# Optimization experiments

Measured on AMD Instinct MI355X. Metric: run time of the kernel, lower is better.

## Reference

```python
import jax, jax.numpy as jnp
import numpy as np

B, T, F, U, L, C = 1024, 100, 300, 512, 2, 10
EPS = 1e-3  # keras LayerNormalization default epsilon


def _ln(z, g, b):
    m = jnp.mean(z, axis=-1, keepdims=True)
    v = jnp.var(z, axis=-1, keepdims=True)
    return (z - m) * jax.lax.rsqrt(v + EPS) * g + b


def _cell(xt, h, c, W, R, bias, kg, kb, rg, rb, sg, sb):
    # LayerNormLSTMCell: LN(x@W) + LN(h@R) + b, gates i,f,g,o; LN on new cell state
    z = _ln(xt @ W, kg, kb) + _ln(h @ R, rg, rb) + bias
    i, f, g, o = jnp.split(z, 4, axis=-1)
    c_new = jax.nn.sigmoid(f) * c + jax.nn.sigmoid(i) * jnp.tanh(g)
    c_new = _ln(c_new, sg, sb)
    h_new = jax.nn.sigmoid(o) * jnp.tanh(c_new)
    return h_new, c_new


def setup_inputs() -> dict:
    key = jax.random.key(0)
    ks = jax.random.split(key, 8 + 2 * L)
    d = {}
    d["x"] = jax.random.normal(ks[0], (B, T, F), jnp.float32)
    lens = jax.random.randint(ks[1], (B,), 1, T + 1)
    d["mask"] = (jnp.arange(T)[None, :] < lens[:, None]).astype(jnp.int32)
    in_dims = [F, U]
    ki = 2
    for l in range(L):
        s = 1.0 / np.sqrt(in_dims[l])
        d[f"W{l}"] = jax.random.uniform(ks[ki], (in_dims[l], 4 * U), jnp.float32, -s, s); ki += 1
        d[f"R{l}"] = jax.random.uniform(ks[ki], (U, 4 * U), jnp.float32, -0.044, 0.044); ki += 1
        d[f"b{l}"] = jnp.zeros((4 * U,), jnp.float32)
        d[f"kg{l}"] = jnp.ones((4 * U,), jnp.float32)
        d[f"kb{l}"] = jnp.zeros((4 * U,), jnp.float32)
        d[f"rg{l}"] = jnp.ones((4 * U,), jnp.float32)
        d[f"rb{l}"] = jnp.zeros((4 * U,), jnp.float32)
        d[f"sg{l}"] = jnp.ones((U,), jnp.float32)
        d[f"sb{l}"] = jnp.zeros((U,), jnp.float32)
    s = 1.0 / np.sqrt(U)
    d["Wd"] = jax.random.uniform(ks[ki], (U, C), jnp.float32, -s, s)
    d["bd"] = jnp.zeros((C,), jnp.float32)
    return d


def _forward(x, mask,
             W0, R0, b0, kg0, kb0, rg0, rb0, sg0, sb0,
             W1, R1, b1, kg1, kb1, rg1, rb1, sg1, sb1,
             Wd, bd):
    params = [
        (W0, R0, b0, kg0, kb0, rg0, rb0, sg0, sb0),
        (W1, R1, b1, kg1, kb1, rg1, rb1, sg1, sb1),
    ]
    bsz = x.shape[0]
    dt = x.dtype

    def step(carry, inp_t):
        states, out_prev = carry
        xt, mt = inp_t  # xt: [B,F], mt: [B] bool
        mb = mt[:, None]
        inp = xt
        new_states = []
        for (h, c), p in zip(states, params):
            hn, cn = _cell(inp, h, c, *p)
            inp = hn
            # Keras RNN masking: carry previous state at masked steps
            new_states.append((jnp.where(mb, hn, h), jnp.where(mb, cn, c)))
        out = jnp.where(mb, inp, out_prev)
        return (tuple(new_states), out), None

    init_states = tuple((jnp.zeros((bsz, U), dt), jnp.zeros((bsz, U), dt)) for _ in range(L))
    carry0 = (init_states, jnp.zeros((bsz, U), dt))
    xs = (jnp.transpose(x, (1, 0, 2)), mask.T.astype(bool))  # time-major
    (_, out), _ = jax.lax.scan(step, carry0, xs)
    return jax.nn.softmax(out @ Wd + bd, axis=-1)


def reference(x, mask,
              W0, R0, b0, kg0, kb0, rg0, rb0, sg0, sb0,
              W1, R1, b1, kg1, kb1, rg1, rb1, sg1, sb1,
              Wd, bd):
    return _forward(x, mask,
                    W0, R0, b0, kg0, kb0, rg0, rb0, sg0, sb0,
                    W1, R1, b1, kg1, kb1, rg1, rb1, sg1, sb1,
                    Wd, bd)
```

## Files before the change

kernel.cpp:

```cpp
#include <hip/hip_runtime.h>

#define B_ 1024
#define T_ 100
#define F_ 300
#define FP_ 320
#define U_ 512
#define G4_ 2048
#define C_ 10
#define EPS_ 1e-3f

typedef _Float16 f16x8 __attribute__((ext_vector_type(8)));
typedef float f32x4 __attribute__((ext_vector_type(4)));

typedef __attribute__((address_space(1))) const void* gcptr_t;
typedef __attribute__((address_space(3))) void* lptr_t;

__device__ __forceinline__ void async_ld16(_Float16* lds, const _Float16* g) {
  __builtin_amdgcn_global_load_lds((gcptr_t)g, (lptr_t)lds, 16, 0, 0);
}

__global__ __launch_bounds__(1024) void prep_kernel(const int* __restrict__ mask,
                                                    int* __restrict__ perm,
                                                    int* __restrict__ nt) {
  __shared__ int cnt[T_ + 1];
  __shared__ int start[T_ + 1];
  int b = threadIdx.x;
  if (b <= T_) cnt[b] = 0;
  __syncthreads();
  const int* mrow = mask + (size_t)b * T_;
  int len = 0;
  for (int t = 0; t < T_; t++) len += mrow[t];
  atomicAdd(&cnt[len], 1);
  __syncthreads();
  if (b == 0) {
    int run = 0;
    for (int l = T_; l >= 0; l--) {
      start[l] = run;
      run += cnt[l];
    }
  }
  __syncthreads();
  if (b < T_) nt[b] = start[b];
  __syncthreads();
  int pos = atomicAdd(&start[len], 1);
  perm[pos] = b;
}


__global__ __launch_bounds__(256) void cast_x_kernel(const float* __restrict__ x,
                                                     const int* __restrict__ perm,
                                                     const int* __restrict__ nt,
                                                     _Float16* __restrict__ xhi,
                                                     _Float16* __restrict__ xlo) {
  size_t cidx = (size_t)blockIdx.x * 256 + threadIdx.x;
  int fc = (int)(cidx % (FP_ / 8));
  size_t bt = cidx / (FP_ / 8);
  int i = (int)(bt % B_);
  int t = (int)(bt / B_);
  int nr = (nt[t] + 127) & ~127;
  if (i >= nr) return;
  int b = perm[i];
  int f = fc * 8;
  const float* xr = x + ((size_t)b * T_ + t) * F_;
  float v[8];
  if (f + 8 <= F_) {
    float4 a = *(const float4*)(xr + f);
    float4 c = *(const float4*)(xr + f + 4);
    v[0] = a.x; v[1] = a.y; v[2] = a.z; v[3] = a.w;
    v[4] = c.x; v[5] = c.y; v[6] = c.z; v[7] = c.w;
  } else {
#pragma unroll
    for (int j = 0; j < 8; j++) v[j] = (f + j < F_) ? xr[f + j] : 0.f;
  }
  f16x8 hi, lo;
#pragma unroll
  for (int j = 0; j < 8; j++) {
    _Float16 h = (_Float16)v[j];
    hi[j] = h;
    lo[j] = (_Float16)(v[j] - (float)h);
  }
  *(f16x8*)(xhi + cidx * 8) = hi;
  *(f16x8*)(xlo + cidx * 8) = lo;
}

__global__ __launch_bounds__(256) void cast_w_kernel(const float* __restrict__ W,
                                                     _Float16* __restrict__ Whi,
                                                     _Float16* __restrict__ Wlo,
                                                     int K, int N, int Kp) {
  __shared__ float tile[32][33];
  int n0 = blockIdx.x * 32, k0 = blockIdx.y * 32;
  int tx = threadIdx.x & 31, ty = threadIdx.x >> 5;
#pragma unroll
  for (int r = 0; r < 32; r += 8) {
    int k = k0 + ty + r;
    tile[ty + r][tx] = (k < K) ? W[(size_t)k * N + n0 + tx] : 0.f;
  }
  __syncthreads();
#pragma unroll
  for (int r = 0; r < 32; r += 8) {
    int n = n0 + ty + r, kk = k0 + tx;
    if (kk < Kp) {
      float v = tile[tx][ty + r];
      _Float16 h = (_Float16)v;
      Whi[(size_t)n * Kp + kk] = h;
      Wlo[(size_t)n * Kp + kk] = (_Float16)(v - (float)h);
    }
  }
}

struct GemmOp {
  const _Float16* A;
  const _Float16* Bt;
  float* G;
  int lda;
  int K;
  size_t aLo;
  int step;
};
struct G4Pack {
  GemmOp op[4];
  const int* nt;
};

__global__ __launch_bounds__(256) void gemm_phase(G4Pack P) {
  GemmOp op = P.op[blockIdx.z];
  const int mBase = blockIdx.y * 128, nBase = blockIdx.x * 128;
  if (mBase >= P.nt[op.step]) return;
  const int K = op.K, lda = op.lda;
  const _Float16* Ah = op.A;
  const _Float16* Al = op.A + op.aLo;
  const _Float16* Bh = op.Bt;
  const _Float16* Bl = op.Bt + (size_t)G4_ * K;

  __shared__ __align__(16) _Float16 ash[128][64];
  __shared__ __align__(16) _Float16 asl[128][64];
  __shared__ __align__(16) _Float16 bsh[128][64];
  __shared__ __align__(16) _Float16 bsl[128][64];

  const int tid = threadIdx.x;
  const int w = tid >> 6;
  const int lane = tid & 63;
  const int wm = (w & 1) << 6;
  const int wn = (w >> 1) << 6;

  f32x4 acc[4][4];
#pragma unroll
  for (int mt = 0; mt < 4; mt++)
#pragma unroll
    for (int nt2 = 0; nt2 < 4; nt2++) acc[mt][nt2] = (f32x4){0.f, 0.f, 0.f, 0.f};

#pragma unroll 1
  for (int k0 = 0; k0 < K; k0 += 64) {
#pragma unroll
    for (int j = 0; j < 4; j++) {
      int i = (w << 2) + j;
      int idx = (i << 6) + lane;
      int row = idx >> 3;
      int cl = ((idx & 7) ^ (row & 7)) << 3;
      size_t aoff = (size_t)(mBase + row) * lda + k0 + cl;
      size_t boff = (size_t)(nBase + row) * K + k0 + cl;
      async_ld16(&ash[0][0] + (i << 9), Ah + aoff);
      async_ld16(&asl[0][0] + (i << 9), Al + aoff);
      async_ld16(&bsh[0][0] + (i << 9), Bh + boff);
      async_ld16(&bsl[0][0] + (i << 9), Bl + boff);
    }
    __syncthreads();
#pragma unroll
    for (int q = 0; q < 2; q++) {
      f16x8 afh[4], afl[4], bfh[4], bfl[4];
#pragma unroll
      for (int mt = 0; mt < 4; mt++) {
        int row = wm + (mt << 4) + (lane & 15);
        int p = ((q << 2) + (lane >> 4)) ^ (row & 7);
        afh[mt] = *(const f16x8*)&ash[row][p << 3];
        afl[mt] = *(const f16x8*)&asl[row][p << 3];
      }
#pragma unroll
      for (int nt2 = 0; nt2 < 4; nt2++) {
        int row = wn + (nt2 << 4) + (lane & 15);
        int p = ((q << 2) + (lane >> 4)) ^ (row & 7);
        bfh[nt2] = *(const f16x8*)&bsh[row][p << 3];
        bfl[nt2] = *(const f16x8*)&bsl[row][p << 3];
      }
      __builtin_amdgcn_s_setprio(1);
#pragma unroll
      for (int mt = 0; mt < 4; mt++)
#pragma unroll
        for (int nt2 = 0; nt2 < 4; nt2++) {
          acc[mt][nt2] = __builtin_amdgcn_mfma_f32_16x16x32_f16(afh[mt], bfh[nt2], acc[mt][nt2], 0, 0, 0);
          acc[mt][nt2] = __builtin_amdgcn_mfma_f32_16x16x32_f16(afl[mt], bfh[nt2], acc[mt][nt2], 0, 0, 0);
          acc[mt][nt2] = __builtin_amdgcn_mfma_f32_16x16x32_f16(afh[mt], bfl[nt2], acc[mt][nt2], 0, 0, 0);
        }
      __builtin_amdgcn_s_setprio(0);
    }
    __syncthreads();
  }
  int q4 = lane >> 4, c = lane & 15;
  float* G = op.G;
#pragma unroll
  for (int mt = 0; mt < 4; mt++)
#pragma unroll
    for (int nt2 = 0; nt2 < 4; nt2++)
#pragma unroll
      for (int r = 0; r < 4; r++) {
        int row = mBase + wm + (mt << 4) + (q4 << 2) + r;
        int col = nBase + wn + (nt2 << 4) + c;
        G[(size_t)row * G4_ + col] = acc[mt][nt2][r];
      }
}


__device__ __forceinline__ void block_reduce(float* v, int n, float* sred, int tid) {
  int lane = tid & 63, w = tid >> 6;
  for (int off = 32; off > 0; off >>= 1)
    for (int i = 0; i < n; i++) v[i] += __shfl_down(v[i], off, 64);
  if (lane == 0)
    for (int i = 0; i < n; i++) sred[w * 4 + i] = v[i];
  __syncthreads();
  if (tid == 0)
    for (int i = 0; i < n; i++) sred[16 + i] = sred[i] + sred[4 + i] + sred[8 + i] + sred[12 + i];
  __syncthreads();
  for (int i = 0; i < n; i++) v[i] = sred[16 + i];
}

__device__ __forceinline__ float sigm(float x) { return 1.f / (1.f + expf(-x)); }

struct CellOp {
  const float* Gx;
  const float* Gh;
  const float* bias;
  const float* kg;
  const float* kb;
  const float* rg;
  const float* rb;
  const float* sg;
  const float* sb;
  float* cS;
  _Float16* hP;
  _Float16* hnP;
  float* outb;
  int step;
};
struct C2Pack {
  CellOp op[2];
  const int* nt;
};

__global__ __launch_bounds__(256) void cell_phase(C2Pack P) {
  CellOp cp = P.op[blockIdx.x >> 10];
  int b = blockIdx.x & (B_ - 1);
  if (b >= P.nt[cp.step]) return;
  int tid = threadIdx.x;
  __shared__ float sred[20];
  const float* gx = cp.Gx + (size_t)b * G4_;
  const float* gh = cp.Gh + (size_t)b * G4_;
  float vx[8], vh[8];
  float s[4] = {0.f, 0.f, 0.f, 0.f};
#pragma unroll
  for (int i = 0; i < 8; i++) {
    int col = tid + (i << 8);
    float a = gx[col], d = gh[col];
    vx[i] = a;
    vh[i] = d;
    s[0] += a;
    s[1] += a * a;
    s[2] += d;
    s[3] += d * d;
  }
  block_reduce(s, 4, sred, tid);
  const float inv = 1.f / 2048.f;
  float m1 = s[0] * inv, m2 = s[2] * inv;
  float rs1 = rsqrtf(fmaxf(s[1] * inv - m1 * m1, 0.f) + EPS_);
  float rs2 = rsqrtf(fmaxf(s[3] * inv - m2 * m2, 0.f) + EPS_);
  float z[8];
#pragma unroll
  for (int i = 0; i < 8; i++) {
    int col = tid + (i << 8);
    z[i] = (vx[i] - m1) * rs1 * cp.kg[col] + cp.kb[col] +
           (vh[i] - m2) * rs2 * cp.rg[col] + cp.rb[col] + cp.bias[col];
  }
  int j0 = tid, j1 = tid + 256;
  size_t base = (size_t)b * U_;
  _Float16* hHi = cp.hP;
  _Float16* hLo = cp.hP + (size_t)B_ * U_;
  float co0 = cp.cS[base + j0], co1 = cp.cS[base + j1];
  float cn0 = sigm(z[2]) * co0 + sigm(z[0]) * tanhf(z[4]);
  float cn1 = sigm(z[3]) * co1 + sigm(z[1]) * tanhf(z[5]);
  float t2[2] = {cn0 + cn1, cn0 * cn0 + cn1 * cn1};
  block_reduce(t2, 2, sred, tid);
  const float invU = 1.f / 512.f;
  float mc = t2[0] * invU;
  float rsc = rsqrtf(fmaxf(t2[1] * invU - mc * mc, 0.f) + EPS_);
  float cl0 = (cn0 - mc) * rsc * cp.sg[j0] + cp.sb[j0];
  float cl1 = (cn1 - mc) * rsc * cp.sg[j1] + cp.sb[j1];
  float hn0 = sigm(z[6]) * tanhf(cl0);
  float hn1 = sigm(z[7]) * tanhf(cl1);
  _Float16 hh0 = (_Float16)hn0, hh1 = (_Float16)hn1;
  hHi[base + j0] = hh0;
  hLo[base + j0] = (_Float16)(hn0 - (float)hh0);
  hHi[base + j1] = hh1;
  hLo[base + j1] = (_Float16)(hn1 - (float)hh1);
  cp.cS[base + j0] = cl0;
  cp.cS[base + j1] = cl1;
  if (cp.hnP) {
    _Float16* nHi = cp.hnP;
    _Float16* nLo = cp.hnP + (size_t)B_ * U_;
    nHi[base + j0] = hh0;
    nLo[base + j0] = (_Float16)(hn0 - (float)hh0);
    nHi[base + j1] = hh1;
    nLo[base + j1] = (_Float16)(hn1 - (float)hh1);
  }
  if (cp.outb) {
    cp.outb[base + j0] = hn0;
    cp.outb[base + j1] = hn1;
  }
}

__global__ __launch_bounds__(64) void dense_softmax_kernel(const float* __restrict__ outb,
                                                           const float* __restrict__ Wd,
                                                           const float* __restrict__ bd,
                                                           const int* __restrict__ perm,
                                                           float* __restrict__ o) {
  int b = blockIdx.x, lane = threadIdx.x;
  __shared__ float sl[16];
  int col = lane & 15, kg = lane >> 4;
  float acc = 0.f;
  if (col < C_) {
    for (int k = kg; k < U_; k += 4) acc += outb[(size_t)b * U_ + k] * Wd[(size_t)k * C_ + col];
  }
  acc += __shfl_down(acc, 16, 64);
  acc += __shfl_down(acc, 32, 64);
  if (lane < C_) sl[lane] = acc + bd[lane];
  __syncthreads();
  if (lane < C_) {
    float mx = sl[0];
    for (int i = 1; i < C_; i++) mx = fmaxf(mx, sl[i]);
    float ssum = 0.f;
    for (int i = 0; i < C_; i++) ssum += expf(sl[i] - mx);
    o[(size_t)perm[b] * C_ + lane] = expf(sl[lane] - mx) / ssum;
  }
}


extern "C" void kernel_launch(void* const* d_in, const int* in_sizes, int n_in,
                              void* d_out, int out_size, void* d_ws, size_t ws_size,
                              hipStream_t stream) {
  const float* x = (const float*)d_in[0];
  const int* mask = (const int*)d_in[1];
  const float* W0 = (const float*)d_in[2];
  const float* R0 = (const float*)d_in[3];
  const float* b0 = (const float*)d_in[4];
  const float* kg0 = (const float*)d_in[5];
  const float* kb0 = (const float*)d_in[6];
  const float* rg0 = (const float*)d_in[7];
  const float* rb0 = (const float*)d_in[8];
  const float* sg0 = (const float*)d_in[9];
  const float* sb0 = (const float*)d_in[10];
  const float* W1 = (const float*)d_in[11];
  const float* R1 = (const float*)d_in[12];
  const float* b1 = (const float*)d_in[13];
  const float* kg1 = (const float*)d_in[14];
  const float* kb1 = (const float*)d_in[15];
  const float* rg1 = (const float*)d_in[16];
  const float* rb1 = (const float*)d_in[17];
  const float* sg1 = (const float*)d_in[18];
  const float* sb1 = (const float*)d_in[19];
  const float* Wd = (const float*)d_in[20];
  const float* bd = (const float*)d_in[21];
  float* out = (float*)d_out;

  char* w = (char*)d_ws;
  size_t o = 0;
  auto alloc = [&](size_t bytes) {
    size_t r = o;
    o += (bytes + 255) & ~(size_t)255;
    return r;
  };
  size_t o_c0s = alloc((size_t)B_ * U_ * 4);
  size_t o_c1s = alloc((size_t)B_ * U_ * 4);
  size_t o_outf = alloc((size_t)B_ * U_ * 4);
  size_t o_h0p = alloc((size_t)B_ * U_ * 2 * 2);
  size_t o_h1p = alloc((size_t)B_ * U_ * 2 * 2);
  size_t o_G0h = alloc((size_t)B_ * G4_ * 4);
  size_t zero_bytes = o;
  size_t o_hn0p = alloc((size_t)B_ * U_ * 2 * 2);
  size_t o_xh = alloc((size_t)T_ * B_ * FP_ * 2 * 2);
  size_t o_W0t = alloc((size_t)G4_ * FP_ * 2 * 2);
  size_t o_R0t = alloc((size_t)G4_ * U_ * 2 * 2);
  size_t o_W1t = alloc((size_t)G4_ * U_ * 2 * 2);
  size_t o_R1t = alloc((size_t)G4_ * U_ * 2 * 2);
  size_t o_G0x = alloc((size_t)B_ * G4_ * 4);
  size_t o_G1x = alloc((size_t)B_ * G4_ * 4);
  size_t o_G1h = alloc((size_t)B_ * G4_ * 4);
  size_t o_perm = alloc((size_t)B_ * 4);
  size_t o_nt = alloc((size_t)T_ * 4);
  (void)ws_size;

  float* c0s = (float*)(w + o_c0s);
  float* c1s = (float*)(w + o_c1s);
  float* outf = (float*)(w + o_outf);
  _Float16* h0p = (_Float16*)(w + o_h0p);
  _Float16* h1p = (_Float16*)(w + o_h1p);
  float* G0h = (float*)(w + o_G0h);
  _Float16* hn0p = (_Float16*)(w + o_hn0p);
  _Float16* xh = (_Float16*)(w + o_xh);
  _Float16* W0t = (_Float16*)(w + o_W0t);
  _Float16* R0t = (_Float16*)(w + o_R0t);
  _Float16* W1t = (_Float16*)(w + o_W1t);
  _Float16* R1t = (_Float16*)(w + o_R1t);
  float* G0x = (float*)(w + o_G0x);
  float* G1x = (float*)(w + o_G1x);
  float* G1h = (float*)(w + o_G1h);
  int* perm = (int*)(w + o_perm);
  int* ntp = (int*)(w + o_nt);

  hipMemsetAsync(w, 0, zero_bytes, stream);

  prep_kernel<<<1, 1024, 0, stream>>>(mask, perm, ntp);

  {
    size_t chunks = (size_t)T_ * B_ * (FP_ / 8);
    cast_x_kernel<<<dim3((unsigned)(chunks / 256)), 256, 0, stream>>>(
        x, perm, ntp, xh, xh + (size_t)T_ * B_ * FP_);
  }
  cast_w_kernel<<<dim3(G4_ / 32, FP_ / 32), 256, 0, stream>>>(
      W0, W0t, W0t + (size_t)G4_ * FP_, F_, G4_, FP_);
  cast_w_kernel<<<dim3(G4_ / 32, U_ / 32), 256, 0, stream>>>(
      R0, R0t, R0t + (size_t)G4_ * U_, U_, G4_, U_);
  cast_w_kernel<<<dim3(G4_ / 32, U_ / 32), 256, 0, stream>>>(
      W1, W1t, W1t + (size_t)G4_ * U_, U_, G4_, U_);
  cast_w_kernel<<<dim3(G4_ / 32, U_ / 32), 256, 0, stream>>>(
      R1, R1t, R1t + (size_t)G4_ * U_, U_, G4_, U_);

  const size_t xLoOff = (size_t)T_ * B_ * FP_;
  const size_t hLoOff = (size_t)B_ * U_;

  auto xw_op = [&](int t) -> GemmOp {
    return GemmOp{xh + (size_t)t * B_ * FP_, W0t, G0x, FP_, FP_, xLoOff, t};
  };
  CellOp cell0op = {G0x, G0h, b0, kg0, kb0, rg0, rb0, sg0, sb0,
                    c0s, h0p, hn0p, nullptr, 0};
  CellOp cell1op = {G1x, G1h, b1, kg1, kb1, rg1, rb1, sg1, sb1,
                    c1s, h1p, nullptr, outf, 0};

  {
    G4Pack P;
    P.nt = ntp;
    P.op[0] = xw_op(0);
    P.op[1] = P.op[0];
    P.op[2] = P.op[0];
    P.op[3] = P.op[0];
    gemm_phase<<<dim3(G4_ / 128, B_ / 128, 1), 256, 0, stream>>>(P);
    C2Pack CP;
    CP.nt = ntp;
    cell0op.step = 0;
    CP.op[0] = cell0op;
    CP.op[1] = cell0op;
    cell_phase<<<B_, 256, 0, stream>>>(CP);
  }

  for (int t = 0; t < T_; t++) {
    bool more = (t < T_ - 1);
    G4Pack P;
    P.nt = ntp;
    P.op[0] = GemmOp{hn0p, W1t, G1x, U_, U_, hLoOff, t};
    P.op[1] = GemmOp{h1p, R1t, G1h, U_, U_, hLoOff, t};
    if (more) {
      P.op[2] = GemmOp{h0p, R0t, G0h, U_, U_, hLoOff, t + 1};
      P.op[3] = xw_op(t + 1);
    } else {
      P.op[2] = P.op[0];
      P.op[3] = P.op[0];
    }
    gemm_phase<<<dim3(G4_ / 128, B_ / 128, more ? 4 : 2), 256, 0, stream>>>(P);

    C2Pack CP;
    CP.nt = ntp;
    cell1op.step = t;
    CP.op[0] = cell1op;
    cell0op.step = t + 1;
    CP.op[1] = more ? cell0op : cell1op;
    cell_phase<<<more ? 2 * B_ : B_, 256, 0, stream>>>(CP);
  }

  dense_softmax_kernel<<<B_, 64, 0, stream>>>(outf, Wd, bd, perm, out);
}
```

Measured before the change: 3.612 ms.

## Double-buffer GEMM LDS tiles with 512 threads and drop duplicate h0 copy

The GEMM kernel moves to 512-thread blocks, each wave owning a 64x32 output slice, and double-buffers the LDS tiles so the async global-to-LDS loads for the next K chunk are issued before computing the current one. LDS use doubles to 128KB per block, which with launch bounds (512,1) limits occupancy to one block per CU. Separately, the layer-0 cell no longer writes a second copy of h into hn0p, and the layer-1 input GEMM reads h0p directly. That removes redundant stores but relies on h0p holding the correct step's hidden state when both GEMMs read it.

```diff
diff --git a/kernel.cpp b/kernel.cpp
--- a/kernel.cpp
+++ b/kernel.cpp
@@ -122,7 +122,7 @@
   const int* nt;
 };
 
-__global__ __launch_bounds__(256) void gemm_phase(G4Pack P) {
+__global__ __launch_bounds__(512, 1) void gemm_phase(G4Pack P) {
   GemmOp op = P.op[blockIdx.z];
   const int mBase = blockIdx.y * 128, nBase = blockIdx.x * 128;
   if (mBase >= P.nt[op.step]) return;
@@ -132,61 +132,73 @@
   const _Float16* Bh = op.Bt;
   const _Float16* Bl = op.Bt + (size_t)G4_ * K;
 
-  __shared__ __align__(16) _Float16 ash[128][64];
-  __shared__ __align__(16) _Float16 asl[128][64];
-  __shared__ __align__(16) _Float16 bsh[128][64];
-  __shared__ __align__(16) _Float16 bsl[128][64];
+  __shared__ __align__(16) _Float16 lds[2][4][128 * 64];
 
   const int tid = threadIdx.x;
   const int w = tid >> 6;
   const int lane = tid & 63;
   const int wm = (w & 1) << 6;
-  const int wn = (w >> 1) << 6;
-
-  f32x4 acc[4][4];
+  const int wn = (w >> 1) << 5;
+
+  f32x4 acc[4][2];
 #pragma unroll
   for (int mt = 0; mt < 4; mt++)
 #pragma unroll
-    for (int nt2 = 0; nt2 < 4; nt2++) acc[mt][nt2] = (f32x4){0.f, 0.f, 0.f, 0.f};
-
+    for (int nt2 = 0; nt2 < 2; nt2++) acc[mt][nt2] = (f32x4){0.f, 0.f, 0.f, 0.f};
+
+  const int i0 = w << 1;
+
+#define STAGE(BUF, K0)                                                    \
+  do {                                                                    \
+    _Float16* base_ = &lds[BUF][0][0];                                    \
+    _Pragma("unroll") for (int j = 0; j < 2; j++) {                       \
+      int i = i0 + j;                                                     \
+      int idx = (i << 6) + lane;                                          \
+      int row = idx >> 3;                                                 \
+      int cl = ((idx & 7) ^ (row & 7)) << 3;                              \
+      size_t aoff = (size_t)(mBase + row) * lda + (K0) + cl;              \
+      size_t boff = (size_t)(nBase + row) * K + (K0) + cl;                \
+      async_ld16(base_ + (i << 9), Ah + aoff);                            \
+      async_ld16(base_ + 8192 + (i << 9), Al + aoff);                     \
+      async_ld16(base_ + 16384 + (i << 9), Bh + boff);                    \
+      async_ld16(base_ + 24576 + (i << 9), Bl + boff);                    \
+    }                                                                     \
+  } while (0)
+
+  STAGE(0, 0);
+  __syncthreads();
+
+  const int nch = K >> 6;
+  int cur = 0;
 #pragma unroll 1
-  for (int k0 = 0; k0 < K; k0 += 64) {
-#pragma unroll
-    for (int j = 0; j < 4; j++) {
-      int i = (w << 2) + j;
-      int idx = (i << 6) + lane;
-      int row = idx >> 3;
-      int cl = ((idx & 7) ^ (row & 7)) << 3;
-      size_t aoff = (size_t)(mBase + row) * lda + k0 + cl;
-      size_t boff = (size_t)(nBase + row) * K + k0 + cl;
-      async_ld16(&ash[0][0] + (i << 9), Ah + aoff);
-      async_ld16(&asl[0][0] + (i << 9), Al + aoff);
-      async_ld16(&bsh[0][0] + (i << 9), Bh + boff);
-      async_ld16(&bsl[0][0] + (i << 9), Bl + boff);
-    }
-    __syncthreads();
+  for (int c = 0; c < nch; c++) {
+    if (c + 1 < nch) STAGE(cur ^ 1, (c + 1) << 6);
+    const _Float16* ash = &lds[cur][0][0];
+    const _Float16* asl = &lds[cur][1][0];
+    const _Float16* bsh = &lds[cur][2][0];
+    const _Float16* bsl = &lds[cur][3][0];
 #pragma unroll
     for (int q = 0; q < 2; q++) {
-      f16x8 afh[4], afl[4], bfh[4], bfl[4];
+      f16x8 afh[4], afl[4], bfh[2], bfl[2];
 #pragma unroll
       for (int mt = 0; mt < 4; mt++) {
         int row = wm + (mt << 4) + (lane & 15);
         int p = ((q << 2) + (lane >> 4)) ^ (row & 7);
-        afh[mt] = *(const f16x8*)&ash[row][p << 3];
-        afl[mt] = *(const f16x8*)&asl[row][p << 3];
+        afh[mt] = *(const f16x8*)&ash[(row << 6) + (p << 3)];
+        afl[mt] = *(const f16x8*)&asl[(row << 6) + (p << 3)];
       }
 #pragma unroll
-      for (int nt2 = 0; nt2 < 4; nt2++) {
+      for (int nt2 = 0; nt2 < 2; nt2++) {
         int row = wn + (nt2 << 4) + (lane & 15);
         int p = ((q << 2) + (lane >> 4)) ^ (row & 7);
-        bfh[nt2] = *(const f16x8*)&bsh[row][p << 3];
-        bfl[nt2] = *(const f16x8*)&bsl[row][p << 3];
+        bfh[nt2] = *(const f16x8*)&bsh[(row << 6) + (p << 3)];
+        bfl[nt2] = *(const f16x8*)&bsl[(row << 6) + (p << 3)];
       }
       __builtin_amdgcn_s_setprio(1);
 #pragma unroll
       for (int mt = 0; mt < 4; mt++)
 #pragma unroll
-        for (int nt2 = 0; nt2 < 4; nt2++) {
+        for (int nt2 = 0; nt2 < 2; nt2++) {
           acc[mt][nt2] = __builtin_amdgcn_mfma_f32_16x16x32_f16(afh[mt], bfh[nt2], acc[mt][nt2], 0, 0, 0);
           acc[mt][nt2] = __builtin_amdgcn_mfma_f32_16x16x32_f16(afl[mt], bfh[nt2], acc[mt][nt2], 0, 0, 0);
           acc[mt][nt2] = __builtin_amdgcn_mfma_f32_16x16x32_f16(afh[mt], bfl[nt2], acc[mt][nt2], 0, 0, 0);
@@ -194,17 +206,20 @@
       __builtin_amdgcn_s_setprio(0);
     }
     __syncthreads();
-  }
-  int q4 = lane >> 4, c = lane & 15;
+    cur ^= 1;
+  }
+#undef STAGE
+
+  int q4 = lane >> 4, cc = lane & 15;
   float* G = op.G;
 #pragma unroll
   for (int mt = 0; mt < 4; mt++)
 #pragma unroll
-    for (int nt2 = 0; nt2 < 4; nt2++)
+    for (int nt2 = 0; nt2 < 2; nt2++)
 #pragma unroll
       for (int r = 0; r < 4; r++) {
         int row = mBase + wm + (mt << 4) + (q4 << 2) + r;
-        int col = nBase + wn + (nt2 << 4) + c;
+        int col = nBase + wn + (nt2 << 4) + cc;
         G[(size_t)row * G4_ + col] = acc[mt][nt2][r];
       }
 }
@@ -237,7 +252,6 @@
   const float* sb;
   float* cS;
   _Float16* hP;
-  _Float16* hnP;
   float* outb;
   int step;
 };
@@ -302,14 +316,6 @@
   hLo[base + j1] = (_Float16)(hn1 - (float)hh1);
   cp.cS[base + j0] = cl0;
   cp.cS[base + j1] = cl1;
-  if (cp.hnP) {
-    _Float16* nHi = cp.hnP;
-    _Float16* nLo = cp.hnP + (size_t)B_ * U_;
-    nHi[base + j0] = hh0;
-    nLo[base + j0] = (_Float16)(hn0 - (float)hh0);
-    nHi[base + j1] = hh1;
-    nLo[base + j1] = (_Float16)(hn1 - (float)hh1);
-  }
   if (cp.outb) {
     cp.outb[base + j0] = hn0;
     cp.outb[base + j1] = hn1;
@@ -383,7 +389,6 @@
   size_t o_h1p = alloc((size_t)B_ * U_ * 2 * 2);
   size_t o_G0h = alloc((size_t)B_ * G4_ * 4);
   size_t zero_bytes = o;
-  size_t o_hn0p = alloc((size_t)B_ * U_ * 2 * 2);
   size_t o_xh = alloc((size_t)T_ * B_ * FP_ * 2 * 2);
   size_t o_W0t = alloc((size_t)G4_ * FP_ * 2 * 2);
   size_t o_R0t = alloc((size_t)G4_ * U_ * 2 * 2);
@@ -402,7 +407,6 @@
   _Float16* h0p = (_Float16*)(w + o_h0p);
   _Float16* h1p = (_Float16*)(w + o_h1p);
   float* G0h = (float*)(w + o_G0h);
-  _Float16* hn0p = (_Float16*)(w + o_hn0p);
   _Float16* xh = (_Float16*)(w + o_xh);
   _Float16* W0t = (_Float16*)(w + o_W0t);
   _Float16* R0t = (_Float16*)(w + o_R0t);
@@ -439,9 +443,9 @@
     return GemmOp{xh + (size_t)t * B_ * FP_, W0t, G0x, FP_, FP_, xLoOff, t};
   };
   CellOp cell0op = {G0x, G0h, b0, kg0, kb0, rg0, rb0, sg0, sb0,
-                    c0s, h0p, hn0p, nullptr, 0};
+                    c0s, h0p, nullptr, 0};
   CellOp cell1op = {G1x, G1h, b1, kg1, kb1, rg1, rb1, sg1, sb1,
-                    c1s, h1p, nullptr, outf, 0};
+                    c1s, h1p, outf, 0};
 
   {
     G4Pack P;
@@ -450,7 +454,7 @@
     P.op[1] = P.op[0];
     P.op[2] = P.op[0];
     P.op[3] = P.op[0];
-    gemm_phase<<<dim3(G4_ / 128, B_ / 128, 1), 256, 0, stream>>>(P);
+    gemm_phase<<<dim3(G4_ / 128, B_ / 128, 1), 512, 0, stream>>>(P);
     C2Pack CP;
     CP.nt = ntp;
     cell0op.step = 0;
@@ -463,7 +467,7 @@
     bool more = (t < T_ - 1);
     G4Pack P;
     P.nt = ntp;
-    P.op[0] = GemmOp{hn0p, W1t, G1x, U_, U_, hLoOff, t};
+    P.op[0] = GemmOp{h0p, W1t, G1x, U_, U_, hLoOff, t};
     P.op[1] = GemmOp{h1p, R1t, G1h, U_, U_, hLoOff, t};
     if (more) {
       P.op[2] = GemmOp{h0p, R0t, G0h, U_, U_, hLoOff, t + 1};
@@ -472,7 +476,7 @@
       P.op[2] = P.op[0];
       P.op[3] = P.op[0];
     }
-    gemm_phase<<<dim3(G4_ / 128, B_ / 128, more ? 4 : 2), 256, 0, stream>>>(P);
+    gemm_phase<<<dim3(G4_ / 128, B_ / 128, more ? 4 : 2), 512, 0, stream>>>(P);
 
     C2Pack CP;
     CP.nt = ntp;
```

Measured after the change: 3.397 ms. 1.06x faster.
